# Kernel tuning notes

Hardware: AMD Instinct MI355X
Metric: run time of the kernel (lower is better)

Reference implementation:

```python
import jax, jax.numpy as jnp
import numpy as np

HIDDEN = 128
STATE = 64
ACTION = 16
D_IO = STATE + ACTION  # 80
BATCH = 4096
SEQ_LEN = 512


def setup_inputs() -> dict:
    key = jax.random.key(0)
    ks = jax.random.split(key, 7)
    s = 1.0 / np.sqrt(HIDDEN)
    return {
        "quantized_hn": jax.random.normal(ks[0], (BATCH, HIDDEN), jnp.float32),
        "W_ih": jax.random.uniform(ks[1], (4 * HIDDEN, D_IO), jnp.float32, -s, s),
        "W_hh": jax.random.uniform(ks[2], (4 * HIDDEN, HIDDEN), jnp.float32, -s, s),
        "b_ih": jax.random.uniform(ks[3], (4 * HIDDEN,), jnp.float32, -s, s),
        "b_hh": jax.random.uniform(ks[4], (4 * HIDDEN,), jnp.float32, -s, s),
        "W_fc": jax.random.uniform(ks[5], (D_IO, HIDDEN), jnp.float32, -s, s),
        "b_fc": jax.random.uniform(ks[6], (D_IO,), jnp.float32, -s, s),
        "seq_len": SEQ_LEN,
    }


def reference(quantized_hn, W_ih, W_hh, b_ih, b_hh, W_fc, b_fc, seq_len):
    B, H = quantized_hn.shape
    D = W_fc.shape[0]

    def step(carry, _):
        h, c, x = carry  # h,c: (B,H); x: (B,D)
        # PyTorch LSTM gate order: i, f, g, o
        gates = x @ W_ih.T + b_ih + h @ W_hh.T + b_hh  # (B, 4H)
        i, f, g, o = jnp.split(gates, 4, axis=-1)
        c_new = jax.nn.sigmoid(f) * c + jax.nn.sigmoid(i) * jnp.tanh(g)
        h_new = jax.nn.sigmoid(o) * jnp.tanh(c_new)
        y = h_new @ W_fc.T + b_fc  # (B, D) -> fed back as next input
        return (h_new, c_new, y), y

    h0 = quantized_hn
    c0 = jnp.zeros((B, H), quantized_hn.dtype)
    x0 = jnp.zeros((B, D), quantized_hn.dtype)
    _, ys = jax.lax.scan(step, (h0, c0, x0), None, length=seq_len)
    return jnp.transpose(ys, (1, 0, 2))  # (B, seq_len, D)
```

## Files before the change

kernel.cpp:

```cpp
#include <hip/hip_runtime.h>

typedef __bf16 bf16_t;
typedef __bf16 bf16x4 __attribute__((ext_vector_type(4)));
typedef __bf16 bf16x8 __attribute__((ext_vector_type(8)));
typedef float  f32x4  __attribute__((ext_vector_type(4)));

#define HID    128
#define DIO    80
#define G4     512
#define TSTEP  512
#define BB     16
#define NBATCH 4096
#define NBLK   (NBATCH / BB)
#define HSTR   136

#define NL2E  -1.4426950408889634f
#define P2L2E  2.8853900817779268f

__device__ bf16_t g_weff_frags[128 * 512];
__device__ bf16_t g_whh_frags[128 * 512];
__device__ bf16_t g_wfc_frags[20 * 512];
__device__ float  g_weff[G4 * HID];
__device__ float  g_beff[G4];
__device__ float  g_b1[G4];

__global__ void k_weff(const float* __restrict__ W_ih, const float* __restrict__ W_hh,
                       const float* __restrict__ b_ih, const float* __restrict__ b_hh,
                       const float* __restrict__ W_fc, const float* __restrict__ b_fc) {
  int gid = blockIdx.x * blockDim.x + threadIdx.x;
  int g = gid >> 7, k = gid & 127;
  float sc = ((g >> 7) == 2) ? P2L2E : NL2E;
  float acc = W_hh[g * HID + k];
#pragma unroll 8
  for (int d = 0; d < DIO; ++d)
    acc = fmaf(W_ih[g * DIO + d], W_fc[d * HID + k], acc);
  g_weff[g * HID + k] = acc * sc;
  if (k == 0) {
    float bb = b_ih[g] + b_hh[g];
    g_b1[g] = bb * sc;
    float be = bb;
    for (int d = 0; d < DIO; ++d) be = fmaf(W_ih[g * DIO + d], b_fc[d], be);
    g_beff[g] = be * sc;
  }
}

__global__ void k_frag(const float* __restrict__ W_hh, const float* __restrict__ W_fc) {
  int tile = blockIdx.x;
  int lane = threadIdx.x;
  int c = lane & 15, q = lane >> 4;
  if (tile < 128) {
    int gtile = tile >> 2, kt = tile & 3;
    int n = gtile * 16 + c;
#pragma unroll
    for (int j = 0; j < 8; ++j)
      g_weff_frags[tile * 512 + lane * 8 + j] = (bf16_t)g_weff[n * HID + kt * 32 + q * 8 + j];
  } else if (tile < 256) {
    int t2 = tile - 128;
    int gtile = t2 >> 2, kt = t2 & 3;
    int n = gtile * 16 + c;
    float sc = ((n >> 7) == 2) ? P2L2E : NL2E;
#pragma unroll
    for (int j = 0; j < 8; ++j)
      g_whh_frags[t2 * 512 + lane * 8 + j] = (bf16_t)(W_hh[n * HID + kt * 32 + q * 8 + j] * sc);
  } else {
    int t2 = tile - 256;
    int yt = t2 >> 2, kt = t2 & 3;
    int n = yt * 16 + c;
#pragma unroll
    for (int j = 0; j < 8; ++j)
      g_wfc_frags[t2 * 512 + lane * 8 + j] = (bf16_t)W_fc[n * HID + kt * 32 + q * 8 + j];
  }
}

__device__ __forceinline__ float fexp2(float x) { return __builtin_amdgcn_exp2f(x); }
__device__ __forceinline__ float frcp(float x)  { return __builtin_amdgcn_rcpf(x); }

__global__ __launch_bounds__(512, 2) void k_lstm(const float* __restrict__ h0,
                                                 const float* __restrict__ b_fc,
                                                 float* __restrict__ out) {
  __shared__ __align__(16) bf16_t hbuf[2][BB * HSTR];
  const int tid = threadIdx.x;
  const int lane = tid & 63;
  const int w = tid >> 6;
  const int c = lane & 15, q = lane >> 4;
  const int b0 = blockIdx.x * BB;

  for (int i = tid; i < BB * HID; i += 512) {
    int r = i >> 7, k = i & 127;
    hbuf[0][r * HSTR + k] = (bf16_t)h0[(long)(b0 + r) * HID + k];
  }

  bf16x8 Wy[4];
  f32x4  ybias;
  if (w < 5) {
#pragma unroll
    for (int kt = 0; kt < 4; ++kt)
      Wy[kt] = *(const bf16x8*)&g_wfc_frags[(w * 4 + kt) * 512 + lane * 8];
#pragma unroll
    for (int r = 0; r < 4; ++r) ybias[r] = b_fc[w * 16 + q * 4 + r];
  }

  bf16x8 Wg[4][4];
  f32x4  bias[4];
  auto load_wg = [&](const bf16_t* frags, const float* bsrc) {
#pragma unroll
    for (int G = 0; G < 4; ++G) {
      int gtile = G * 8 + w;
#pragma unroll
      for (int r = 0; r < 4; ++r) bias[G][r] = bsrc[gtile * 16 + q * 4 + r];
#pragma unroll
      for (int kt = 0; kt < 4; ++kt)
        Wg[G][kt] = *(const bf16x8*)&frags[(gtile * 4 + kt) * 512 + lane * 8];
    }
  };

  f32x4 cst = (f32x4){0, 0, 0, 0};
  bf16x8 hfA[4], hfB[4];

  __syncthreads();
#pragma unroll
  for (int kt = 0; kt < 4; ++kt)
    hfA[kt] = *(const bf16x8*)&hbuf[0][c * HSTR + kt * 32 + q * 8];

  float* outp = out + (long)(b0 + c) * TSTEP * DIO + w * 16 + q * 4;

  if (((tid >> 6) & 1) == 0) __builtin_amdgcn_s_setprio(1);

#define ITER(CUR, NXT, BUF, EMIT)                                                      \
  do {                                                                                 \
    f32x4 acc[4];                                                                      \
    _Pragma("unroll")                                                                  \
    for (int G = 0; G < 4; ++G)                                                        \
      acc[G] = __builtin_amdgcn_mfma_f32_16x16x32_bf16(Wg[G][0], CUR[0], bias[G], 0, 0, 0); \
    _Pragma("unroll")                                                                  \
    for (int kt = 1; kt < 4; ++kt)                                                     \
      _Pragma("unroll")                                                                \
      for (int G = 0; G < 4; ++G)                                                      \
        acc[G] = __builtin_amdgcn_mfma_f32_16x16x32_bf16(Wg[G][kt], CUR[kt], acc[G], 0, 0, 0); \
    bf16x4 hv;                                                                         \
    _Pragma("unroll")                                                                  \
    for (int r = 0; r < 4; ++r) {                                                      \
      float Ei = fexp2(acc[0][r]);                                           \
      float Ef = fexp2(acc[1][r]);                                           \
      float Eg = fexp2(acc[2][r]);                                           \
      float Eo = fexp2(acc[3][r]);                                           \
      float ai = 1.0f + Ei, af = 1.0f + Ef, ag = 1.0f + Eg;                            \
      float P1 = ai * ag;                                                              \
      float R  = frcp(P1 * af);                                                        \
      float tg = __builtin_fmaf(Eg, P2L2E, -P2L2E);                     \
      float m2 = tg * af;                                                              \
      float u  = __builtin_fmaf(P1, cst[r], m2);                                       \
      float cn = u * R;                            \
      cst[r] = cn;                                                                     \
      float cc = fminf(cn, 80.0f);                            \
      float Ec = fexp2(cc);                                                  \
      float R2 = frcp((1.0f + Eo) * (1.0f + Ec));                                      \
      hv[r] = (bf16_t)((Ec - 1.0f) * R2);                          \
    }                                                                                  \
    *(bf16x4*)&hbuf[BUF][c * HSTR + w * 16 + q * 4] = hv;                              \
    __syncthreads();                                                                   \
    _Pragma("unroll")                                                                  \
    for (int kt = 0; kt < 4; ++kt)                                                     \
      NXT[kt] = *(const bf16x8*)&hbuf[BUF][c * HSTR + kt * 32 + q * 8];                \
    if (EMIT && w < 5) {  \
      f32x4 ya = __builtin_amdgcn_mfma_f32_16x16x32_bf16(Wy[0], CUR[0], ybias, 0, 0, 0); \
      _Pragma("unroll")                                                                \
      for (int kt = 1; kt < 4; ++kt)                                                   \
        ya = __builtin_amdgcn_mfma_f32_16x16x32_bf16(Wy[kt], CUR[kt], ya, 0, 0, 0);    \
      *(f32x4*)outp = ya;                                                              \
      outp += DIO;                                                                     \
    }                                                                                  \
  } while (0)

  load_wg(g_whh_frags, g_b1);
  ITER(hfA, hfB, 1, false);
  load_wg(g_weff_frags, g_beff);
  for (int p = 0; p < 255; ++p) {
    ITER(hfB, hfA, 0, true);
    ITER(hfA, hfB, 1, true);
  }
  ITER(hfB, hfA, 0, true);

  if (w < 5) {
    f32x4 ya = __builtin_amdgcn_mfma_f32_16x16x32_bf16(Wy[0], hfA[0], ybias, 0, 0, 0);
#pragma unroll
    for (int kt = 1; kt < 4; ++kt)
      ya = __builtin_amdgcn_mfma_f32_16x16x32_bf16(Wy[kt], hfA[kt], ya, 0, 0, 0);
    *(f32x4*)outp = ya;
  }
#undef ITER
}

extern "C" void kernel_launch(void* const* d_in, const int* in_sizes, int n_in,
                              void* d_out, int out_size, void* d_ws, size_t ws_size,
                              hipStream_t stream) {
  const float* h0   = (const float*)d_in[0];
  const float* W_ih = (const float*)d_in[1];
  const float* W_hh = (const float*)d_in[2];
  const float* b_ih = (const float*)d_in[3];
  const float* b_hh = (const float*)d_in[4];
  const float* W_fc = (const float*)d_in[5];
  const float* b_fc = (const float*)d_in[6];
  float* out = (float*)d_out;

  k_weff<<<256, 256, 0, stream>>>(W_ih, W_hh, b_ih, b_hh, W_fc, b_fc);
  k_frag<<<276, 64, 0, stream>>>(W_hh, W_fc);
  k_lstm<<<NBLK, 512, 0, stream>>>(h0, b_fc, out);
}
```

Measured before the change: 931.7 us.

## Halve waves per block, give each wave two gate tiles and interleave MFMA with tail math

Each block now runs 4 waves instead of 8, and each wave computes two column tiles of all four gates. The activation tail of the first tile is interleaved with the MFMAs of the second, with sched_group_barrier hints to overlap matrix and VALU work. The FC output work is redistributed so wave 0 also handles the fifth tile. This doubles register use per wave and lowers occupancy (launch bounds 256,1), and it drops the setprio hint, in exchange for fewer waves contending at the per-step barrier and better MFMA/VALU overlap.

```diff
diff --git a/kernel.cpp b/kernel.cpp
--- a/kernel.cpp
+++ b/kernel.cpp
@@ -75,7 +75,32 @@
 __device__ __forceinline__ float fexp2(float x) { return __builtin_amdgcn_exp2f(x); }
 __device__ __forceinline__ float frcp(float x)  { return __builtin_amdgcn_rcpf(x); }
 
-__global__ __launch_bounds__(512, 2) void k_lstm(const float* __restrict__ h0,
+#define MFMA16(A, B, C) __builtin_amdgcn_mfma_f32_16x16x32_bf16((A), (B), (C), 0, 0, 0)
+#define SGB(m, n) __builtin_amdgcn_sched_group_barrier((m), (n), 0)
+
+#define TAILR(AI, AF, AG, AO, CST, HV, R)                                              \
+  do {                                                                                 \
+    float Eg = fexp2(AG[R]);                                                 \
+    float ag = 1.0f + Eg;                                                              \
+    float Ei = fexp2(AI[R]);                                                 \
+    float ai = 1.0f + Ei;                                                              \
+    float Ef = fexp2(AF[R]);                                                 \
+    float af = 1.0f + Ef;                                                              \
+    float P1 = ai * ag;                                                                \
+    float Rr = frcp(P1 * af);                                                          \
+    float tg = __builtin_fmaf(Eg, P2L2E, -P2L2E);                       \
+    float m2 = tg * af;                                                                \
+    float u  = __builtin_fmaf(P1, CST[R], m2);                                         \
+    float cn = u * Rr;                             \
+    CST[R] = cn;                                                                       \
+    float cc = fminf(cn, 80.0f);                              \
+    float Ec = fexp2(cc);                                                    \
+    float Eo = fexp2(AO[R]);                                                 \
+    float R2 = frcp((1.0f + Eo) * (1.0f + Ec));                                        \
+    HV[R] = (bf16_t)((Ec - 1.0f) * R2);                            \
+  } while (0)
+
+__global__ __launch_bounds__(256, 1) void k_lstm(const float* __restrict__ h0,
                                                  const float* __restrict__ b_fc,
                                                  float* __restrict__ out) {
   __shared__ __align__(16) bf16_t hbuf[2][BB * HSTR];
@@ -85,36 +110,44 @@
   const int c = lane & 15, q = lane >> 4;
   const int b0 = blockIdx.x * BB;
 
-  for (int i = tid; i < BB * HID; i += 512) {
+  for (int i = tid; i < BB * HID; i += 256) {
     int r = i >> 7, k = i & 127;
     hbuf[0][r * HSTR + k] = (bf16_t)h0[(long)(b0 + r) * HID + k];
   }
 
-  bf16x8 Wy[4];
-  f32x4  ybias;
-  if (w < 5) {
+  bf16x8 Wy0[4], Wy4[4];
+  f32x4  yb0, yb4;
+#pragma unroll
+  for (int kt = 0; kt < 4; ++kt)
+    Wy0[kt] = *(const bf16x8*)&g_wfc_frags[(w * 4 + kt) * 512 + lane * 8];
+#pragma unroll
+  for (int r = 0; r < 4; ++r) yb0[r] = b_fc[w * 16 + q * 4 + r];
+  if (w == 0) {
 #pragma unroll
     for (int kt = 0; kt < 4; ++kt)
-      Wy[kt] = *(const bf16x8*)&g_wfc_frags[(w * 4 + kt) * 512 + lane * 8];
-#pragma unroll
-    for (int r = 0; r < 4; ++r) ybias[r] = b_fc[w * 16 + q * 4 + r];
-  }
-
-  bf16x8 Wg[4][4];
-  f32x4  bias[4];
+      Wy4[kt] = *(const bf16x8*)&g_wfc_frags[(4 * 4 + kt) * 512 + lane * 8];
+#pragma unroll
+    for (int r = 0; r < 4; ++r) yb4[r] = b_fc[4 * 16 + q * 4 + r];
+  }
+
+  bf16x8 Wg[2][4][4];
+  f32x4  bias[2][4];
   auto load_wg = [&](const bf16_t* frags, const float* bsrc) {
 #pragma unroll
-    for (int G = 0; G < 4; ++G) {
-      int gtile = G * 8 + w;
-#pragma unroll
-      for (int r = 0; r < 4; ++r) bias[G][r] = bsrc[gtile * 16 + q * 4 + r];
-#pragma unroll
-      for (int kt = 0; kt < 4; ++kt)
-        Wg[G][kt] = *(const bf16x8*)&frags[(gtile * 4 + kt) * 512 + lane * 8];
-    }
+    for (int U = 0; U < 2; ++U)
+#pragma unroll
+      for (int G = 0; G < 4; ++G) {
+        int gtile = G * 8 + (2 * w + U);
+#pragma unroll
+        for (int r = 0; r < 4; ++r) bias[U][G][r] = bsrc[gtile * 16 + q * 4 + r];
+#pragma unroll
+        for (int kt = 0; kt < 4; ++kt)
+          Wg[U][G][kt] = *(const bf16x8*)&frags[(gtile * 4 + kt) * 512 + lane * 8];
+      }
   };
 
-  f32x4 cst = (f32x4){0, 0, 0, 0};
+  f32x4 cst0 = (f32x4){0, 0, 0, 0};
+  f32x4 cst1 = (f32x4){0, 0, 0, 0};
   bf16x8 hfA[4], hfB[4];
 
   __syncthreads();
@@ -122,53 +155,85 @@
   for (int kt = 0; kt < 4; ++kt)
     hfA[kt] = *(const bf16x8*)&hbuf[0][c * HSTR + kt * 32 + q * 8];
 
-  float* outp = out + (long)(b0 + c) * TSTEP * DIO + w * 16 + q * 4;
-
-  if (((tid >> 6) & 1) == 0) __builtin_amdgcn_s_setprio(1);
+  float* outp0 = out + (long)(b0 + c) * TSTEP * DIO + w * 16 + q * 4;
+  float* outp4 = out + (long)(b0 + c) * TSTEP * DIO + 64 + q * 4;
 
 #define ITER(CUR, NXT, BUF, EMIT)                                                      \
   do {                                                                                 \
-    f32x4 acc[4];                                                                      \
-    _Pragma("unroll")                                                                  \
-    for (int G = 0; G < 4; ++G)                                                        \
-      acc[G] = __builtin_amdgcn_mfma_f32_16x16x32_bf16(Wg[G][0], CUR[0], bias[G], 0, 0, 0); \
-    _Pragma("unroll")                                                                  \
-    for (int kt = 1; kt < 4; ++kt)                                                     \
-      _Pragma("unroll")                                                                \
-      for (int G = 0; G < 4; ++G)                                                      \
-        acc[G] = __builtin_amdgcn_mfma_f32_16x16x32_bf16(Wg[G][kt], CUR[kt], acc[G], 0, 0, 0); \
-    bf16x4 hv;                                                                         \
-    _Pragma("unroll")                                                                  \
-    for (int r = 0; r < 4; ++r) {                                                      \
-      float Ei = fexp2(acc[0][r]);                                           \
-      float Ef = fexp2(acc[1][r]);                                           \
-      float Eg = fexp2(acc[2][r]);                                           \
-      float Eo = fexp2(acc[3][r]);                                           \
-      float ai = 1.0f + Ei, af = 1.0f + Ef, ag = 1.0f + Eg;                            \
-      float P1 = ai * ag;                                                              \
-      float R  = frcp(P1 * af);                                                        \
-      float tg = __builtin_fmaf(Eg, P2L2E, -P2L2E);                     \
-      float m2 = tg * af;                                                              \
-      float u  = __builtin_fmaf(P1, cst[r], m2);                                       \
-      float cn = u * R;                            \
-      cst[r] = cn;                                                                     \
-      float cc = fminf(cn, 80.0f);                            \
-      float Ec = fexp2(cc);                                                  \
-      float R2 = frcp((1.0f + Eo) * (1.0f + Ec));                                      \
-      hv[r] = (bf16_t)((Ec - 1.0f) * R2);                          \
-    }                                                                                  \
-    *(bf16x4*)&hbuf[BUF][c * HSTR + w * 16 + q * 4] = hv;                              \
+    f32x4 aI0, aF0, aG0, aO0, aI1, aF1, aG1, aO1;                                      \
+    bf16x4 hv0, hv1;                                                                   \
+                                  \
+    aI0 = MFMA16(Wg[0][0][0], CUR[0], bias[0][0]);                                     \
+    aF0 = MFMA16(Wg[0][1][0], CUR[0], bias[0][1]);                                     \
+    aG0 = MFMA16(Wg[0][2][0], CUR[0], bias[0][2]);                                     \
+    aO0 = MFMA16(Wg[0][3][0], CUR[0], bias[0][3]);                                     \
+    aI0 = MFMA16(Wg[0][0][1], CUR[1], aI0);                                            \
+    aF0 = MFMA16(Wg[0][1][1], CUR[1], aF0);                                            \
+    aG0 = MFMA16(Wg[0][2][1], CUR[1], aG0);                                            \
+    aO0 = MFMA16(Wg[0][3][1], CUR[1], aO0);                                            \
+    aI0 = MFMA16(Wg[0][0][2], CUR[2], aI0);                                            \
+    aF0 = MFMA16(Wg[0][1][2], CUR[2], aF0);                                            \
+    aG0 = MFMA16(Wg[0][2][2], CUR[2], aG0);                                            \
+    aO0 = MFMA16(Wg[0][3][2], CUR[2], aO0);                                            \
+    aI0 = MFMA16(Wg[0][0][3], CUR[3], aI0);                                            \
+    aF0 = MFMA16(Wg[0][1][3], CUR[3], aF0);                                            \
+    aG0 = MFMA16(Wg[0][2][3], CUR[3], aG0);                                            \
+    aO0 = MFMA16(Wg[0][3][3], CUR[3], aO0);                                            \
+     \
+    aI1 = MFMA16(Wg[1][0][0], CUR[0], bias[1][0]);                                     \
+    aF1 = MFMA16(Wg[1][1][0], CUR[0], bias[1][1]);                                     \
+    aG1 = MFMA16(Wg[1][2][0], CUR[0], bias[1][2]);                                     \
+    aO1 = MFMA16(Wg[1][3][0], CUR[0], bias[1][3]);                                     \
+    TAILR(aI0, aF0, aG0, aO0, cst0, hv0, 0);                                           \
+    aI1 = MFMA16(Wg[1][0][1], CUR[1], aI1);                                            \
+    aF1 = MFMA16(Wg[1][1][1], CUR[1], aF1);                                            \
+    aG1 = MFMA16(Wg[1][2][1], CUR[1], aG1);                                            \
+    aO1 = MFMA16(Wg[1][3][1], CUR[1], aO1);                                            \
+    TAILR(aI0, aF0, aG0, aO0, cst0, hv0, 1);                                           \
+    aI1 = MFMA16(Wg[1][0][2], CUR[2], aI1);                                            \
+    aF1 = MFMA16(Wg[1][1][2], CUR[2], aF1);                                            \
+    aG1 = MFMA16(Wg[1][2][2], CUR[2], aG1);                                            \
+    aO1 = MFMA16(Wg[1][3][2], CUR[2], aO1);                                            \
+    TAILR(aI0, aF0, aG0, aO0, cst0, hv0, 2);                                           \
+    aI1 = MFMA16(Wg[1][0][3], CUR[3], aI1);                                            \
+    aF1 = MFMA16(Wg[1][1][3], CUR[3], aF1);                                            \
+    aG1 = MFMA16(Wg[1][2][3], CUR[3], aG1);                                            \
+    aO1 = MFMA16(Wg[1][3][3], CUR[3], aO1);                                            \
+    TAILR(aI0, aF0, aG0, aO0, cst0, hv0, 3);                                           \
+                                                                          \
+    TAILR(aI1, aF1, aG1, aO1, cst1, hv1, 0);                                           \
+    TAILR(aI1, aF1, aG1, aO1, cst1, hv1, 1);                                           \
+    TAILR(aI1, aF1, aG1, aO1, cst1, hv1, 2);                                           \
+    TAILR(aI1, aF1, aG1, aO1, cst1, hv1, 3);                                           \
+    *(bf16x4*)&hbuf[BUF][c * HSTR + (2 * w) * 16 + q * 4]     = hv0;                   \
+    *(bf16x4*)&hbuf[BUF][c * HSTR + (2 * w + 1) * 16 + q * 4] = hv1;                   \
+     \
+    SGB(0x008, 16);                                                                    \
+    SGB(0x008, 4); SGB(0x002, 24);                                                     \
+    SGB(0x008, 4); SGB(0x002, 24);                                                     \
+    SGB(0x008, 4); SGB(0x002, 24);                                                     \
+    SGB(0x008, 4); SGB(0x002, 24);                                                     \
+    SGB(0x002, 96);                                                                    \
+    SGB(0x200, 2);                                                                     \
     __syncthreads();                                                                   \
     _Pragma("unroll")                                                                  \
     for (int kt = 0; kt < 4; ++kt)                                                     \
       NXT[kt] = *(const bf16x8*)&hbuf[BUF][c * HSTR + kt * 32 + q * 8];                \
-    if (EMIT && w < 5) {  \
-      f32x4 ya = __builtin_amdgcn_mfma_f32_16x16x32_bf16(Wy[0], CUR[0], ybias, 0, 0, 0); \
-      _Pragma("unroll")                                                                \
-      for (int kt = 1; kt < 4; ++kt)                                                   \
-        ya = __builtin_amdgcn_mfma_f32_16x16x32_bf16(Wy[kt], CUR[kt], ya, 0, 0, 0);    \
-      *(f32x4*)outp = ya;                                                              \
-      outp += DIO;                                                                     \
+    if (EMIT) {      \
+      f32x4 ya = MFMA16(Wy0[0], CUR[0], yb0);                                          \
+      ya = MFMA16(Wy0[1], CUR[1], ya);                                                 \
+      ya = MFMA16(Wy0[2], CUR[2], ya);                                                 \
+      ya = MFMA16(Wy0[3], CUR[3], ya);                                                 \
+      *(f32x4*)outp0 = ya;                                                             \
+      outp0 += DIO;                                                                    \
+      if (w == 0) {                                                                    \
+        f32x4 yc = MFMA16(Wy4[0], CUR[0], yb4);                                        \
+        yc = MFMA16(Wy4[1], CUR[1], yc);                                               \
+        yc = MFMA16(Wy4[2], CUR[2], yc);                                               \
+        yc = MFMA16(Wy4[3], CUR[3], yc);                                               \
+        *(f32x4*)outp4 = yc;                                                           \
+        outp4 += DIO;                                                                  \
+      }                                                                                \
     }                                                                                  \
   } while (0)
 
@@ -181,12 +246,19 @@
   }
   ITER(hfB, hfA, 0, true);
 
-  if (w < 5) {
-    f32x4 ya = __builtin_amdgcn_mfma_f32_16x16x32_bf16(Wy[0], hfA[0], ybias, 0, 0, 0);
-#pragma unroll
-    for (int kt = 1; kt < 4; ++kt)
-      ya = __builtin_amdgcn_mfma_f32_16x16x32_bf16(Wy[kt], hfA[kt], ya, 0, 0, 0);
-    *(f32x4*)outp = ya;
+  {
+    f32x4 ya = MFMA16(Wy0[0], hfA[0], yb0);
+    ya = MFMA16(Wy0[1], hfA[1], ya);
+    ya = MFMA16(Wy0[2], hfA[2], ya);
+    ya = MFMA16(Wy0[3], hfA[3], ya);
+    *(f32x4*)outp0 = ya;
+    if (w == 0) {
+      f32x4 yc = MFMA16(Wy4[0], hfA[0], yb4);
+      yc = MFMA16(Wy4[1], hfA[1], yc);
+      yc = MFMA16(Wy4[2], hfA[2], yc);
+      yc = MFMA16(Wy4[3], hfA[3], yc);
+      *(f32x4*)outp4 = yc;
+    }
   }
 #undef ITER
 }
@@ -205,5 +277,5 @@
 
   k_weff<<<256, 256, 0, stream>>>(W_ih, W_hh, b_ih, b_hh, W_fc, b_fc);
   k_frag<<<276, 64, 0, stream>>>(W_hh, W_fc);
-  k_lstm<<<NBLK, 512, 0, stream>>>(h0, b_fc, out);
-}
+  k_lstm<<<NBLK, 256, 0, stream>>>(h0, b_fc, out);
+}
```

Result: slower. 997.8 us (+7.1%).

## Split LSTM step into half-K phases with staggered gate-tail computation across warp halves

Applied to the files above, without the earlier changes.

Restructures the recurrent loop so each step is split into two phases around a mid-step barrier: the first half of the hidden vector (k-tiles 0-1) written by low warps is consumed while high warps are still finishing their activation tail, and the second half arrives after the barrier. Low and high warp groups compute their gate nonlinearities at different points, overlapping MFMA work on one half of h with transcendental work on the other. The output projection is moved between the two halves to fill gaps. This adds a second barrier per step and more complex prologue/epilogue, risking extra sync overhead if the overlap doesn't materialise.

```diff
diff --git a/kernel.cpp b/kernel.cpp
--- a/kernel.cpp
+++ b/kernel.cpp
@@ -75,6 +75,30 @@
 __device__ __forceinline__ float fexp2(float x) { return __builtin_amdgcn_exp2f(x); }
 __device__ __forceinline__ float frcp(float x)  { return __builtin_amdgcn_rcpf(x); }
 
+#define MFMA16(A, B, C) __builtin_amdgcn_mfma_f32_16x16x32_bf16((A), (B), (C), 0, 0, 0)
+
+#define TAILR(ACC, CST, HV, R)                                                         \
+  do {                                                                                 \
+    float Eg = fexp2(ACC[2][R]);                                             \
+    float ag = 1.0f + Eg;                                                              \
+    float Ei = fexp2(ACC[0][R]);                                             \
+    float ai = 1.0f + Ei;                                                              \
+    float Ef = fexp2(ACC[1][R]);                                             \
+    float af = 1.0f + Ef;                                                              \
+    float P1 = ai * ag;                                                                \
+    float Rr = frcp(P1 * af);                                                          \
+    float tg = __builtin_fmaf(Eg, P2L2E, -P2L2E);                       \
+    float m2 = tg * af;                                                                \
+    float u  = __builtin_fmaf(P1, CST[R], m2);                                         \
+    float cn = u * Rr;                             \
+    CST[R] = cn;                                                                       \
+    float cc = fminf(cn, 80.0f);                              \
+    float Ec = fexp2(cc);                                                    \
+    float Eo = fexp2(ACC[3][R]);                                             \
+    float R2 = frcp((1.0f + Eo) * (1.0f + Ec));                                        \
+    HV[R] = (bf16_t)((Ec - 1.0f) * R2);                            \
+  } while (0)
+
 __global__ __launch_bounds__(512, 2) void k_lstm(const float* __restrict__ h0,
                                                  const float* __restrict__ b_fc,
                                                  float* __restrict__ out) {
@@ -84,6 +108,7 @@
   const int w = tid >> 6;
   const int c = lane & 15, q = lane >> 4;
   const int b0 = blockIdx.x * BB;
+  const bool isHigh = (w >= 4);
 
   for (int i = tid; i < BB * HID; i += 512) {
     int r = i >> 7, k = i & 127;
@@ -116,79 +141,125 @@
 
   f32x4 cst = (f32x4){0, 0, 0, 0};
   bf16x8 hfA[4], hfB[4];
-
-  __syncthreads();
+  f32x4 accA[4], accB[4];
+
+  __syncthreads();
+
 #pragma unroll
   for (int kt = 0; kt < 4; ++kt)
     hfA[kt] = *(const bf16x8*)&hbuf[0][c * HSTR + kt * 32 + q * 8];
-
+  load_wg(g_whh_frags, g_b1);
+#pragma unroll
+  for (int G = 0; G < 4; ++G) accB[G] = MFMA16(Wg[G][0], hfA[0], bias[G]);
+#pragma unroll
+  for (int kt = 1; kt < 4; ++kt)
+#pragma unroll
+    for (int G = 0; G < 4; ++G) accB[G] = MFMA16(Wg[G][kt], hfA[kt], accB[G]);
+  {
+    bf16x4 hv;
+    TAILR(accB, cst, hv, 0); TAILR(accB, cst, hv, 1);
+    TAILR(accB, cst, hv, 2); TAILR(accB, cst, hv, 3);
+    *(bf16x4*)&hbuf[1][c * HSTR + w * 16 + q * 4] = hv;
+  }
+  __syncthreads();
+
+  load_wg(g_weff_frags, g_beff);
   float* outp = out + (long)(b0 + c) * TSTEP * DIO + w * 16 + q * 4;
 
-  if (((tid >> 6) & 1) == 0) __builtin_amdgcn_s_setprio(1);
-
-#define ITER(CUR, NXT, BUF, EMIT)                                                      \
+  hfB[0] = *(const bf16x8*)&hbuf[1][c * HSTR + 0 * 32 + q * 8];
+  hfB[1] = *(const bf16x8*)&hbuf[1][c * HSTR + 1 * 32 + q * 8];
+#pragma unroll
+  for (int G = 0; G < 4; ++G) accA[G] = MFMA16(Wg[G][0], hfB[0], bias[G]);
+#pragma unroll
+  for (int G = 0; G < 4; ++G) accA[G] = MFMA16(Wg[G][1], hfB[1], accA[G]);
+  hfB[2] = *(const bf16x8*)&hbuf[1][c * HSTR + 2 * 32 + q * 8];
+  hfB[3] = *(const bf16x8*)&hbuf[1][c * HSTR + 3 * 32 + q * 8];
+#pragma unroll
+  for (int G = 0; G < 4; ++G) accA[G] = MFMA16(Wg[G][2], hfB[2], accA[G]);
+#pragma unroll
+  for (int G = 0; G < 4; ++G) accA[G] = MFMA16(Wg[G][3], hfB[3], accA[G]);
+  if (!isHigh) {
+    bf16x4 hv;
+    TAILR(accA, cst, hv, 0); TAILR(accA, cst, hv, 1);
+    TAILR(accA, cst, hv, 2); TAILR(accA, cst, hv, 3);
+    *(bf16x4*)&hbuf[0][c * HSTR + w * 16 + q * 4] = hv;
+  }
+  __syncthreads();
+
+#define STEP(NXT, CUR, ACCB, ACCE, B0, B1)                                             \
   do {                                                                                 \
-    f32x4 acc[4];                                                                      \
-    _Pragma("unroll")                                                                  \
-    for (int G = 0; G < 4; ++G)                                                        \
-      acc[G] = __builtin_amdgcn_mfma_f32_16x16x32_bf16(Wg[G][0], CUR[0], bias[G], 0, 0, 0); \
-    _Pragma("unroll")                                                                  \
-    for (int kt = 1; kt < 4; ++kt)                                                     \
-      _Pragma("unroll")                                                                \
-      for (int G = 0; G < 4; ++G)                                                      \
-        acc[G] = __builtin_amdgcn_mfma_f32_16x16x32_bf16(Wg[G][kt], CUR[kt], acc[G], 0, 0, 0); \
-    bf16x4 hv;                                                                         \
-    _Pragma("unroll")                                                                  \
-    for (int r = 0; r < 4; ++r) {                                                      \
-      float Ei = fexp2(acc[0][r]);                                           \
-      float Ef = fexp2(acc[1][r]);                                           \
-      float Eg = fexp2(acc[2][r]);                                           \
-      float Eo = fexp2(acc[3][r]);                                           \
-      float ai = 1.0f + Ei, af = 1.0f + Ef, ag = 1.0f + Eg;                            \
-      float P1 = ai * ag;                                                              \
-      float R  = frcp(P1 * af);                                                        \
-      float tg = __builtin_fmaf(Eg, P2L2E, -P2L2E);                     \
-      float m2 = tg * af;                                                              \
-      float u  = __builtin_fmaf(P1, cst[r], m2);                                       \
-      float cn = u * R;                            \
-      cst[r] = cn;                                                                     \
-      float cc = fminf(cn, 80.0f);                            \
-      float Ec = fexp2(cc);                                                  \
-      float R2 = frcp((1.0f + Eo) * (1.0f + Ec));                                      \
-      hv[r] = (bf16_t)((Ec - 1.0f) * R2);                          \
+                                                \
+    NXT[0] = *(const bf16x8*)&hbuf[B0][c * HSTR + 0 * 32 + q * 8];                     \
+    NXT[1] = *(const bf16x8*)&hbuf[B0][c * HSTR + 1 * 32 + q * 8];                     \
+    if (isHigh) {                \
+      __builtin_amdgcn_s_setprio(1);                                                   \
+      bf16x4 hv;                                                                       \
+      TAILR(ACCE, cst, hv, 0); TAILR(ACCE, cst, hv, 1);                                \
+      TAILR(ACCE, cst, hv, 2); TAILR(ACCE, cst, hv, 3);                                \
+      *(bf16x4*)&hbuf[B0][c * HSTR + w * 16 + q * 4] = hv;              \
+      __builtin_amdgcn_s_setprio(0);                                                   \
     }                                                                                  \
-    *(bf16x4*)&hbuf[BUF][c * HSTR + w * 16 + q * 4] = hv;                              \
-    __syncthreads();                                                                   \
-    _Pragma("unroll")                                                                  \
-    for (int kt = 0; kt < 4; ++kt)                                                     \
-      NXT[kt] = *(const bf16x8*)&hbuf[BUF][c * HSTR + kt * 32 + q * 8];                \
-    if (EMIT && w < 5) {  \
-      f32x4 ya = __builtin_amdgcn_mfma_f32_16x16x32_bf16(Wy[0], CUR[0], ybias, 0, 0, 0); \
-      _Pragma("unroll")                                                                \
-      for (int kt = 1; kt < 4; ++kt)                                                   \
-        ya = __builtin_amdgcn_mfma_f32_16x16x32_bf16(Wy[kt], CUR[kt], ya, 0, 0, 0);    \
+    _Pragma("unroll")                                                                  \
+    for (int G = 0; G < 4; ++G) ACCB[G] = MFMA16(Wg[G][0], NXT[0], bias[G]);           \
+    _Pragma("unroll")                                                                  \
+    for (int G = 0; G < 4; ++G) ACCB[G] = MFMA16(Wg[G][1], NXT[1], ACCB[G]);           \
+    __syncthreads();                                                     \
+                                               \
+    NXT[2] = *(const bf16x8*)&hbuf[B0][c * HSTR + 2 * 32 + q * 8];                     \
+    NXT[3] = *(const bf16x8*)&hbuf[B0][c * HSTR + 3 * 32 + q * 8];                     \
+    if (w < 5) {                \
+      f32x4 ya = MFMA16(Wy[0], CUR[0], ybias);                                         \
+      ya = MFMA16(Wy[1], CUR[1], ya);                                                  \
+      ya = MFMA16(Wy[2], CUR[2], ya);                                                  \
+      ya = MFMA16(Wy[3], CUR[3], ya);                                                  \
       *(f32x4*)outp = ya;                                                              \
       outp += DIO;                                                                     \
     }                                                                                  \
+    _Pragma("unroll")                                                                  \
+    for (int G = 0; G < 4; ++G) ACCB[G] = MFMA16(Wg[G][2], NXT[2], ACCB[G]);           \
+    _Pragma("unroll")                                                                  \
+    for (int G = 0; G < 4; ++G) ACCB[G] = MFMA16(Wg[G][3], NXT[3], ACCB[G]);           \
+    if (!isHigh) {                                  \
+      __builtin_amdgcn_s_setprio(1);                                                   \
+      bf16x4 hv;                                                                       \
+      TAILR(ACCB, cst, hv, 0); TAILR(ACCB, cst, hv, 1);                                \
+      TAILR(ACCB, cst, hv, 2); TAILR(ACCB, cst, hv, 3);                                \
+      *(bf16x4*)&hbuf[B1][c * HSTR + w * 16 + q * 4] = hv;             \
+      __builtin_amdgcn_s_setprio(0);                                                   \
+    }                                                                                  \
+    __syncthreads();                                                   \
   } while (0)
 
-  load_wg(g_whh_frags, g_b1);
-  ITER(hfA, hfB, 1, false);
-  load_wg(g_weff_frags, g_beff);
   for (int p = 0; p < 255; ++p) {
-    ITER(hfB, hfA, 0, true);
-    ITER(hfA, hfB, 1, true);
-  }
-  ITER(hfB, hfA, 0, true);
-
+    STEP(hfA, hfB, accB, accA, 0, 1);
+    STEP(hfB, hfA, accA, accB, 1, 0);
+  }
+
+  hfA[0] = *(const bf16x8*)&hbuf[0][c * HSTR + 0 * 32 + q * 8];
+  hfA[1] = *(const bf16x8*)&hbuf[0][c * HSTR + 1 * 32 + q * 8];
+  if (isHigh) {
+    bf16x4 hv;
+    TAILR(accA, cst, hv, 0); TAILR(accA, cst, hv, 1);
+    TAILR(accA, cst, hv, 2); TAILR(accA, cst, hv, 3);
+    *(bf16x4*)&hbuf[0][c * HSTR + w * 16 + q * 4] = hv;
+  }
+  __syncthreads();
+  hfA[2] = *(const bf16x8*)&hbuf[0][c * HSTR + 2 * 32 + q * 8];
+  hfA[3] = *(const bf16x8*)&hbuf[0][c * HSTR + 3 * 32 + q * 8];
   if (w < 5) {
-    f32x4 ya = __builtin_amdgcn_mfma_f32_16x16x32_bf16(Wy[0], hfA[0], ybias, 0, 0, 0);
-#pragma unroll
-    for (int kt = 1; kt < 4; ++kt)
-      ya = __builtin_amdgcn_mfma_f32_16x16x32_bf16(Wy[kt], hfA[kt], ya, 0, 0, 0);
+    f32x4 ya = MFMA16(Wy[0], hfB[0], ybias);
+    ya = MFMA16(Wy[1], hfB[1], ya);
+    ya = MFMA16(Wy[2], hfB[2], ya);
+    ya = MFMA16(Wy[3], hfB[3], ya);
     *(f32x4*)outp = ya;
-  }
-#undef ITER
+    outp += DIO;
+    f32x4 yb = MFMA16(Wy[0], hfA[0], ybias);
+    yb = MFMA16(Wy[1], hfA[1], yb);
+    yb = MFMA16(Wy[2], hfA[2], yb);
+    yb = MFMA16(Wy[3], hfA[3], yb);
+    *(f32x4*)outp = yb;
+  }
+#undef STEP
 }
 
 extern "C" void kernel_launch(void* const* d_in, const int* in_sizes, int n_in,
```

After: 962.7 us. 1.03x slower.

## Replace per-step block barrier with LDS flag polling and split-K early start

Applied to the files above, without the earlier changes.

Each step's __syncthreads is replaced by per-wave progress counters in shared memory. Consumer waves spin until the producers of the half of h they need have published, so gate MFMAs on the first K half can start before the other half is ready. Low and high waves take the K halves in opposite orders, and the output projection is interleaved between them. The setprio tweak is removed and the final-step handling is reworked. This adds LDS polling traffic and relies on the volatile-flag ordering being correct.

```diff
diff --git a/kernel.cpp b/kernel.cpp
--- a/kernel.cpp
+++ b/kernel.cpp
@@ -75,20 +75,69 @@
 __device__ __forceinline__ float fexp2(float x) { return __builtin_amdgcn_exp2f(x); }
 __device__ __forceinline__ float frcp(float x)  { return __builtin_amdgcn_rcpf(x); }
 
+#define MFMA16(A, B, C) __builtin_amdgcn_mfma_f32_16x16x32_bf16((A), (B), (C), 0, 0, 0)
+
+#define TAILR(ACC, CST, HV, R)                                                         \
+  do {                                                                                 \
+    float Eg = fexp2(ACC[2][R]);                                             \
+    float ag = 1.0f + Eg;                                                              \
+    float Ei = fexp2(ACC[0][R]);                                             \
+    float ai = 1.0f + Ei;                                                              \
+    float Ef = fexp2(ACC[1][R]);                                             \
+    float af = 1.0f + Ef;                                                              \
+    float P1 = ai * ag;                                                                \
+    float Rr = frcp(P1 * af);                                                          \
+    float tg = __builtin_fmaf(Eg, P2L2E, -P2L2E);                       \
+    float m2 = tg * af;                                                                \
+    float u  = __builtin_fmaf(P1, CST[R], m2);                                         \
+    float cn = u * Rr;                             \
+    CST[R] = cn;                                                                       \
+    float cc = fminf(cn, 80.0f);                              \
+    float Ec = fexp2(cc);                                                    \
+    float Eo = fexp2(ACC[3][R]);                                             \
+    float R2 = frcp((1.0f + Eo) * (1.0f + Ec));                                        \
+    HV[R] = (bf16_t)((Ec - 1.0f) * R2);                            \
+  } while (0)
+
+#define GKT_FIRST(K, SRC)                                                              \
+  acc[0] = MFMA16(Wg[0][K], SRC, bias[0]); acc[1] = MFMA16(Wg[1][K], SRC, bias[1]);    \
+  acc[2] = MFMA16(Wg[2][K], SRC, bias[2]); acc[3] = MFMA16(Wg[3][K], SRC, bias[3]);
+#define GKT(K, SRC)                                                                    \
+  acc[0] = MFMA16(Wg[0][K], SRC, acc[0]); acc[1] = MFMA16(Wg[1][K], SRC, acc[1]);      \
+  acc[2] = MFMA16(Wg[2][K], SRC, acc[2]); acc[3] = MFMA16(Wg[3][K], SRC, acc[3]);
+
+#define YEMIT(PRV)                                                                     \
+  { f32x4 ya = MFMA16(Wy[0], PRV[0], ybias); ya = MFMA16(Wy[1], PRV[1], ya);           \
+    ya = MFMA16(Wy[2], PRV[2], ya); ya = MFMA16(Wy[3], PRV[3], ya);                    \
+    *(f32x4*)outp = ya; outp += DIO; }
+
+__device__ __forceinline__ void poll_ge(volatile unsigned* vf, int base, unsigned need) {
+  for (;;) {
+    unsigned a = vf[base + 0], b = vf[base + 1], x = vf[base + 2], d = vf[base + 3];
+    unsigned m0 = a < b ? a : b, m1 = x < d ? x : d;
+    if ((m0 < m1 ? m0 : m1) >= need) break;
+  }
+  __builtin_amdgcn_sched_barrier(0);
+}
+
 __global__ __launch_bounds__(512, 2) void k_lstm(const float* __restrict__ h0,
                                                  const float* __restrict__ b_fc,
                                                  float* __restrict__ out) {
   __shared__ __align__(16) bf16_t hbuf[2][BB * HSTR];
+  __shared__ unsigned hflags[8];
+  volatile unsigned* vf = hflags;
   const int tid = threadIdx.x;
   const int lane = tid & 63;
   const int w = tid >> 6;
   const int c = lane & 15, q = lane >> 4;
   const int b0 = blockIdx.x * BB;
+  const bool isHigh = (w >= 4);
 
   for (int i = tid; i < BB * HID; i += 512) {
     int r = i >> 7, k = i & 127;
     hbuf[0][r * HSTR + k] = (bf16_t)h0[(long)(b0 + r) * HID + k];
   }
+  if (lane == 0) hflags[w] = 1;
 
   bf16x8 Wy[4];
   f32x4  ybias;
@@ -117,75 +166,76 @@
   f32x4 cst = (f32x4){0, 0, 0, 0};
   bf16x8 hfA[4], hfB[4];
 
+  load_wg(g_whh_frags, g_b1);
   __syncthreads();
+
+  float* outp = out + (long)(b0 + c) * TSTEP * DIO + w * 16 + q * 4;
+
 #pragma unroll
   for (int kt = 0; kt < 4; ++kt)
     hfA[kt] = *(const bf16x8*)&hbuf[0][c * HSTR + kt * 32 + q * 8];
-
-  float* outp = out + (long)(b0 + c) * TSTEP * DIO + w * 16 + q * 4;
-
-  if (((tid >> 6) & 1) == 0) __builtin_amdgcn_s_setprio(1);
-
-#define ITER(CUR, NXT, BUF, EMIT)                                                      \
+  {
+    f32x4 acc[4];
+    GKT_FIRST(0, hfA[0]); GKT(1, hfA[1]); GKT(2, hfA[2]); GKT(3, hfA[3]);
+    bf16x4 hv;
+    TAILR(acc, cst, hv, 0); TAILR(acc, cst, hv, 1);
+    TAILR(acc, cst, hv, 2); TAILR(acc, cst, hv, 3);
+    *(bf16x4*)&hbuf[1][c * HSTR + w * 16 + q * 4] = hv;
+    asm volatile("s_waitcnt lgkmcnt(0)" ::: "memory");
+    if (lane == 0) vf[w] = 2;
+  }
+  load_wg(g_weff_frags, g_beff);
+
+#define ITER(RD, PR, T, EMIT)                                                          \
   do {                                                                                 \
+    const int rb = ((T)-1) & 1, wb = (T)&1;                                            \
     f32x4 acc[4];                                                                      \
-    _Pragma("unroll")                                                                  \
-    for (int G = 0; G < 4; ++G)                                                        \
-      acc[G] = __builtin_amdgcn_mfma_f32_16x16x32_bf16(Wg[G][0], CUR[0], bias[G], 0, 0, 0); \
-    _Pragma("unroll")                                                                  \
-    for (int kt = 1; kt < 4; ++kt)                                                     \
-      _Pragma("unroll")                                                                \
-      for (int G = 0; G < 4; ++G)                                                      \
-        acc[G] = __builtin_amdgcn_mfma_f32_16x16x32_bf16(Wg[G][kt], CUR[kt], acc[G], 0, 0, 0); \
+    if (!isHigh) {                                                                     \
+      poll_ge(vf, 0, (unsigned)(T));                                                   \
+      RD[0] = *(const bf16x8*)&hbuf[rb][c * HSTR + 0 * 32 + q * 8];                    \
+      RD[1] = *(const bf16x8*)&hbuf[rb][c * HSTR + 1 * 32 + q * 8];                    \
+      GKT_FIRST(0, RD[0]); GKT(1, RD[1]);                                              \
+      poll_ge(vf, 4, (unsigned)(T));                                                   \
+      RD[2] = *(const bf16x8*)&hbuf[rb][c * HSTR + 2 * 32 + q * 8];                    \
+      RD[3] = *(const bf16x8*)&hbuf[rb][c * HSTR + 3 * 32 + q * 8];                    \
+      if ((EMIT) && w < 5) YEMIT(PR);                                                  \
+      GKT(2, RD[2]); GKT(3, RD[3]);                                                    \
+    } else {                                                                           \
+      poll_ge(vf, 4, (unsigned)(T));                                                   \
+      RD[2] = *(const bf16x8*)&hbuf[rb][c * HSTR + 2 * 32 + q * 8];                    \
+      RD[3] = *(const bf16x8*)&hbuf[rb][c * HSTR + 3 * 32 + q * 8];                    \
+      GKT_FIRST(2, RD[2]); GKT(3, RD[3]);                                              \
+      poll_ge(vf, 0, (unsigned)(T));                                                   \
+      RD[0] = *(const bf16x8*)&hbuf[rb][c * HSTR + 0 * 32 + q * 8];                    \
+      RD[1] = *(const bf16x8*)&hbuf[rb][c * HSTR + 1 * 32 + q * 8];                    \
+      if ((EMIT) && w < 5) YEMIT(PR);                                                  \
+      GKT(0, RD[0]); GKT(1, RD[1]);                                                    \
+    }                                                                                  \
     bf16x4 hv;                                                                         \
-    _Pragma("unroll")                                                                  \
-    for (int r = 0; r < 4; ++r) {                                                      \
-      float Ei = fexp2(acc[0][r]);                                           \
-      float Ef = fexp2(acc[1][r]);                                           \
-      float Eg = fexp2(acc[2][r]);                                           \
-      float Eo = fexp2(acc[3][r]);                                           \
-      float ai = 1.0f + Ei, af = 1.0f + Ef, ag = 1.0f + Eg;                            \
-      float P1 = ai * ag;                                                              \
-      float R  = frcp(P1 * af);                                                        \
-      float tg = __builtin_fmaf(Eg, P2L2E, -P2L2E);                     \
-      float m2 = tg * af;                                                              \
-      float u  = __builtin_fmaf(P1, cst[r], m2);                                       \
-      float cn = u * R;                            \
-      cst[r] = cn;                                                                     \
-      float cc = fminf(cn, 80.0f);                            \
-      float Ec = fexp2(cc);                                                  \
-      float R2 = frcp((1.0f + Eo) * (1.0f + Ec));                                      \
-      hv[r] = (bf16_t)((Ec - 1.0f) * R2);                          \
-    }                                                                                  \
-    *(bf16x4*)&hbuf[BUF][c * HSTR + w * 16 + q * 4] = hv;                              \
-    __syncthreads();                                                                   \
-    _Pragma("unroll")                                                                  \
-    for (int kt = 0; kt < 4; ++kt)                                                     \
-      NXT[kt] = *(const bf16x8*)&hbuf[BUF][c * HSTR + kt * 32 + q * 8];                \
-    if (EMIT && w < 5) {  \
-      f32x4 ya = __builtin_amdgcn_mfma_f32_16x16x32_bf16(Wy[0], CUR[0], ybias, 0, 0, 0); \
-      _Pragma("unroll")                                                                \
-      for (int kt = 1; kt < 4; ++kt)                                                   \
-        ya = __builtin_amdgcn_mfma_f32_16x16x32_bf16(Wy[kt], CUR[kt], ya, 0, 0, 0);    \
-      *(f32x4*)outp = ya;                                                              \
-      outp += DIO;                                                                     \
-    }                                                                                  \
+    TAILR(acc, cst, hv, 0); TAILR(acc, cst, hv, 1);                                    \
+    TAILR(acc, cst, hv, 2); TAILR(acc, cst, hv, 3);                                    \
+    *(bf16x4*)&hbuf[wb][c * HSTR + w * 16 + q * 4] = hv;                     \
+    asm volatile("s_waitcnt lgkmcnt(0)" ::: "memory");                                 \
+    if (lane == 0) vf[w] = (unsigned)((T) + 1);                                        \
   } while (0)
 
-  load_wg(g_whh_frags, g_b1);
-  ITER(hfA, hfB, 1, false);
-  load_wg(g_weff_frags, g_beff);
+  ITER(hfB, hfA, 2, false);
   for (int p = 0; p < 255; ++p) {
-    ITER(hfB, hfA, 0, true);
-    ITER(hfA, hfB, 1, true);
-  }
-  ITER(hfB, hfA, 0, true);
+    ITER(hfA, hfB, 3 + 2 * p, true);
+    ITER(hfB, hfA, 4 + 2 * p, true);
+  }
 
   if (w < 5) {
-    f32x4 ya = __builtin_amdgcn_mfma_f32_16x16x32_bf16(Wy[0], hfA[0], ybias, 0, 0, 0);
-#pragma unroll
-    for (int kt = 1; kt < 4; ++kt)
-      ya = __builtin_amdgcn_mfma_f32_16x16x32_bf16(Wy[kt], hfA[kt], ya, 0, 0, 0);
+    YEMIT(hfB);
+    poll_ge(vf, 0, 513u);
+    poll_ge(vf, 4, 513u);
+#pragma unroll
+    for (int kt = 0; kt < 4; ++kt)
+      hfA[kt] = *(const bf16x8*)&hbuf[0][c * HSTR + kt * 32 + q * 8];
+    f32x4 ya = MFMA16(Wy[0], hfA[0], ybias);
+    ya = MFMA16(Wy[1], hfA[1], ya);
+    ya = MFMA16(Wy[2], hfA[2], ya);
+    ya = MFMA16(Wy[3], hfA[3], ya);
     *(f32x4*)outp = ya;
   }
 #undef ITER
```

Measured after the change: 1.026 ms. 10.1% more time.
